# Kernel optimization log

Measured on AMD Instinct MI355X. Metric: run time of the kernel, lower is better.

## Reference

```python
import jax, jax.numpy as jnp
import numpy as np

N, S, E, H = 4, 1024, 768, 12
EPS = 1e-5


def layer_norm(x, g, b):
    m = jnp.mean(x, axis=-1, keepdims=True)
    v = jnp.mean((x - m) ** 2, axis=-1, keepdims=True)
    return (x - m) * jax.lax.rsqrt(v + EPS) * g + b


def setup_inputs() -> dict:
    key = jax.random.key(0)
    ks = jax.random.split(key, 18)
    s = 0.02
    return {
        "inputs": jax.random.normal(ks[0], (N, S, E), jnp.float32),
        "g1": jnp.ones((E,), jnp.float32),
        "b1": jnp.zeros((E,), jnp.float32),
        # per-head full-size projections: [H, E, E] (in->out layout)
        "Wq": jax.random.normal(ks[1], (H, E, E), jnp.float32) * s,
        "bq": jax.random.normal(ks[2], (H, E), jnp.float32) * s,
        "Wk": jax.random.normal(ks[3], (H, E, E), jnp.float32) * s,
        "bk": jax.random.normal(ks[4], (H, E), jnp.float32) * s,
        "Wv": jax.random.normal(ks[5], (H, E, E), jnp.float32) * s,
        "bv": jax.random.normal(ks[6], (H, E), jnp.float32) * s,
        "Wc": jax.random.normal(ks[7], (H * E, E), jnp.float32) * s,
        "bc": jax.random.normal(ks[8], (E,), jnp.float32) * s,
        "g2": jnp.ones((E,), jnp.float32),
        "b2": jnp.zeros((E,), jnp.float32),
        "Wfc": jax.random.normal(ks[9], (E, 4 * E), jnp.float32) * s,
        "bfc": jax.random.normal(ks[10], (4 * E,), jnp.float32) * s,
        "Wp": jax.random.normal(ks[11], (4 * E, E), jnp.float32) * s,
        "bp": jax.random.normal(ks[12], (E,), jnp.float32) * s,
    }


def reference(inputs, g1, b1, Wq, bq, Wk, bk, Wv, bv, Wc, bc, g2, b2, Wfc, bfc, Wp, bp):
    x = layer_norm(inputs, g1, b1)  # pre_norm output

    # batched per-head projections: [H, N, S, E]
    q = jnp.einsum('nse,hef->hnsf', x, Wq) + bq[:, None, None, :]
    k = jnp.einsum('nse,hef->hnsf', x, Wk) + bk[:, None, None, :]
    v = jnp.einsum('nse,hef->hnsf', x, Wv) + bv[:, None, None, :]

    # scores scaled by sqrt(n_embed) (as in the source), causal mask, softmax
    scores = jnp.einsum('hnsf,hntf->hnst', q, k) / jnp.sqrt(jnp.float32(E))
    causal = jnp.tril(jnp.ones((S, S), bool))
    scores = jnp.where(causal, scores, jnp.float32(-jnp.inf))
    attn = jax.nn.softmax(scores, axis=-1)
    heads = jnp.einsum('hnst,hntf->hnsf', attn, v)  # [H, N, S, E]

    # concat heads along feature dim -> [N, S, H*E], then c_proj
    cat = jnp.transpose(heads, (1, 2, 0, 3)).reshape(N, S, H * E)
    mha_out = cat @ Wc + bc

    # residual adds the NORMED input (as in the source)
    y = mha_out + x
    y2 = layer_norm(y, g2, b2)

    h = jax.nn.gelu(y2 @ Wfc + bfc, approximate=False)
    mlp_out = h @ Wp + bp
    return mlp_out + y2
```

## Files before the change

kernel.cpp:

```cpp
#include <hip/hip_runtime.h>
#include <hip/hip_bf16.h>
#include <math.h>


#define BM 128
#define BN 128
#define BK 64

typedef __attribute__((ext_vector_type(8))) short bf16x8;
typedef __attribute__((ext_vector_type(4))) float floatx4;

__device__ __forceinline__ short f2b(float f) {
  __hip_bfloat16 h = __float2bfloat16(f);
  return *reinterpret_cast<short*>(&h);
}
__device__ __forceinline__ float b2f(short s) {
  unsigned u = ((unsigned)(unsigned short)s) << 16;
  return __uint_as_float(u);
}

#if defined(__has_builtin)
#if __has_builtin(__builtin_amdgcn_global_load_lds)
#define HAS_GLLD 1
#endif
#endif

#ifdef HAS_GLLD
__device__ __forceinline__ void lds_dma16(const short* g, short* l) {
  __builtin_amdgcn_global_load_lds(
      (const __attribute__((address_space(1))) void*)g,
      (__attribute__((address_space(3))) void*)l, 16, 0, 0);
}
#endif

struct GP {
  const short* A; const short* B;
  long a_bs, b_bs;
  int lda, ldb;
  int a_kh; long a_hs;
  const float* bias0; const float* bias1; const float* bias2;
  short* C0; short* C1; short* C2;
  float* Cf;
  int ldc, zmod;
  long cz0, cz1, c_zs;
  int K, kchunk;
  float alpha;
  int zoff;
};

template<int MODE, int CAUSAL>
__device__ __forceinline__ void gemm_body(const GP& p)
{
  int bx = blockIdx.x;
  if (CAUSAL == 2) bx = gridDim.x - 1 - bx;
  const int m0 = bx * BM, n0 = blockIdx.y * BN;
  if (CAUSAL == 1 && n0 > m0 + (BM - 1)) return;
  const int z = blockIdx.z;
  const short* Ab = p.A + (size_t)z * p.a_bs;
  const short* Bb = p.B + (size_t)z * p.b_bs;
  int kbeg = 0, kend = p.K;
  if (p.kchunk) { kbeg = z * p.kchunk; kend = kbeg + p.kchunk; }
  if (CAUSAL == 2) { int lim = m0 + BM; if (lim < kend) kend = lim; }

  __shared__ __align__(16) short As[BM * BK];
  __shared__ __align__(16) short Bs[BN * BK];

  const int tid = threadIdx.x;
  const int lane = tid & 63, wave = tid >> 6;
  const int wm = (wave >> 1) * 64, wn = (wave & 1) * 64;
  const int l15 = lane & 15, quad = lane >> 4;
  const int rl = lane >> 3, pl = lane & 7;

  floatx4 acc[4][4];
#pragma unroll
  for (int i = 0; i < 4; i++)
#pragma unroll
    for (int j = 0; j < 4; j++) acc[i][j] = (floatx4){0.f, 0.f, 0.f, 0.f};

  const int cs = (pl - rl) & 7;

  for (int k0 = kbeg; k0 < kend; k0 += BK) {
    const short* Ak = Ab; int kb = k0;
    if (p.a_kh) { int h = k0 / p.a_kh; Ak = Ab + (size_t)h * p.a_hs; kb = k0 - h * p.a_kh; }
#pragma unroll
    for (int s = 0; s < 4; s++) {
      const int win = wave * 4 + s;
      const int row = win * 8 + rl;
      const short* ga = Ak + (size_t)(m0 + row) * p.lda + kb + cs * 8;
      const short* gb = Bb + (size_t)(n0 + row) * p.ldb + k0 + cs * 8;
#ifdef HAS_GLLD
      lds_dma16(ga, &As[win * 512]);
      lds_dma16(gb, &Bs[win * 512]);
#else
      *(int4*)&As[win * 512 + lane * 8] = *(const int4*)ga;
      *(int4*)&Bs[win * 512 + lane * 8] = *(const int4*)gb;
#endif
    }
    __syncthreads();
#pragma unroll
    for (int t = 0; t < 2; t++) {
      bf16x8 fa[4], fb[4];
#pragma unroll
      for (int i = 0; i < 4; i++) {
        const int ra = wm + i * 16 + l15;
        fa[i] = *(const bf16x8*)&As[ra * 64 + (((t << 2) + quad + ra) & 7) * 8];
        const int rb = wn + i * 16 + l15;
        fb[i] = *(const bf16x8*)&Bs[rb * 64 + (((t << 2) + quad + rb) & 7) * 8];
      }
#pragma unroll
      for (int i = 0; i < 4; i++)
#pragma unroll
        for (int j = 0; j < 4; j++)
          acc[i][j] = __builtin_amdgcn_mfma_f32_16x16x32_bf16(fa[i], fb[j], acc[i][j], 0, 0, 0);
    }
    __syncthreads();
  }

  const long coff = (long)(z % p.zmod) * p.cz0 + (long)(z / p.zmod) * p.cz1;
#pragma unroll
  for (int j = 0; j < 4; j++) {
    const int col = n0 + wn + j * 16 + l15;
    if constexpr (MODE == 0) {
#pragma unroll
      for (int i = 0; i < 4; i++) {
        const int rb = m0 + wm + i * 16 + quad * 4;
#pragma unroll
        for (int r = 0; r < 4; r++)
          p.C0[coff + (size_t)(rb + r) * p.ldc + col] = f2b(acc[i][j][r] * p.alpha);
      }
    } else if constexpr (MODE == 5) {
      const int part = (n0 + wn) / 768;
      const int cc = col - part * 768;
      const float* bp_ = (part == 0) ? p.bias0 : ((part == 1) ? p.bias1 : p.bias2);
      const float bvv = bp_[(p.zoff + z) * 768 + cc];
      if (part < 2) {
        short* dst = part ? p.C1 : p.C0;
#pragma unroll
        for (int i = 0; i < 4; i++) {
          const int rb = m0 + wm + i * 16 + quad * 4;
#pragma unroll
          for (int r = 0; r < 4; r++)
            dst[(size_t)z * p.c_zs + (size_t)(rb + r) * 768 + cc] = f2b(acc[i][j][r] + bvv);
        }
      } else {
#pragma unroll
        for (int i = 0; i < 4; i++) {
          const int rb = m0 + wm + i * 16 + quad * 4;
          short4 pk;
          pk.x = f2b(acc[i][j][0] + bvv);
          pk.y = f2b(acc[i][j][1] + bvv);
          pk.z = f2b(acc[i][j][2] + bvv);
          pk.w = f2b(acc[i][j][3] + bvv);
          const size_t addr = (((size_t)z * 4 + (rb >> 10)) * 768 + cc) * 1024 + (rb & 1023);
          *(short4*)&p.C2[addr] = pk;
        }
      }
    } else if constexpr (MODE == 4) {
#pragma unroll
      for (int i = 0; i < 4; i++) {
        const int rb = m0 + wm + i * 16 + quad * 4;
#pragma unroll
        for (int r = 0; r < 4; r++)
          p.Cf[(size_t)z * p.c_zs + (size_t)(rb + r) * p.ldc + col] = acc[i][j][r];
      }
    } else {
      const float bvv = p.bias0[col];
#pragma unroll
      for (int i = 0; i < 4; i++) {
        const int rb = m0 + wm + i * 16 + quad * 4;
#pragma unroll
        for (int r = 0; r < 4; r++) {
          float t = acc[i][j][r] + bvv;
          float u = 1.59576912160573071176f * t * (1.0f + 0.044715f * t * t);
          float gl = __fdividef(t, 1.0f + __expf(-u));
          p.C0[(size_t)(rb + r) * p.ldc + col] = f2b(gl);
        }
      }
    }
  }
}

__global__ void __launch_bounds__(256, 4) gemm_qkv(GP p)   { gemm_body<5, 0>(p); }
__global__ void __launch_bounds__(256, 4) gemm_sco(GP p)   { gemm_body<0, 1>(p); }
__global__ void __launch_bounds__(256, 4) gemm_pv(GP p)    { gemm_body<0, 2>(p); }
__global__ void __launch_bounds__(256, 4) gemm_cproj(GP p) { gemm_body<4, 0>(p); }
__global__ void __launch_bounds__(256, 4) gemm_fc(GP p)    { gemm_body<3, 0>(p); }
__global__ void __launch_bounds__(256, 4) gemm_mproj(GP p) { gemm_body<4, 0>(p); }

__global__ void __launch_bounds__(256) ln_kernel(
    const float* __restrict__ in, const float* __restrict__ g, const float* __restrict__ b,
    float* __restrict__ outf, short* __restrict__ outb)
{
  const long r = blockIdx.x;
  const float* x = in + r * 768;
  const int tid = threadIdx.x;
  float v0 = x[tid], v1 = x[tid + 256], v2 = x[tid + 512];
  float s = v0 + v1 + v2;
  float sq = v0 * v0 + v1 * v1 + v2 * v2;
  __shared__ float red[8];
  int lane = tid & 63, wave = tid >> 6;
#pragma unroll
  for (int o = 1; o < 64; o <<= 1) { s += __shfl_xor(s, o); sq += __shfl_xor(sq, o); }
  if (lane == 0) { red[wave] = s; red[4 + wave] = sq; }
  __syncthreads();
  s = red[0] + red[1] + red[2] + red[3];
  sq = red[4] + red[5] + red[6] + red[7];
  float mean = s * (1.0f / 768.0f);
  float var = sq * (1.0f / 768.0f) - mean * mean;
  float inv = rsqrtf(var + 1e-5f);
#pragma unroll
  for (int u = 0; u < 3; u++) {
    int c = tid + u * 256;
    float v = (u == 0) ? v0 : ((u == 1) ? v1 : v2);
    float y = (v - mean) * inv * g[c] + b[c];
    outf[r * 768 + c] = y;
    outb[r * 768 + c] = f2b(y);
  }
}

__global__ void __launch_bounds__(256) reduce_ln_kernel(
    const float* __restrict__ part, long pzs, int nsplit,
    const float* __restrict__ bias, const float* __restrict__ resid,
    const float* __restrict__ g, const float* __restrict__ b,
    float* __restrict__ outf, short* __restrict__ outb)
{
  const long r = blockIdx.x;
  const int tid = threadIdx.x;
  float y[3];
#pragma unroll
  for (int u = 0; u < 3; u++) {
    const int c = tid + u * 256;
    const size_t idx = (size_t)r * 768 + c;
    float s = part[idx];
    for (int zz = 1; zz < nsplit; zz++) s += part[(size_t)zz * pzs + idx];
    y[u] = s + bias[c] + resid[idx];
  }
  float s = y[0] + y[1] + y[2];
  float sq = y[0] * y[0] + y[1] * y[1] + y[2] * y[2];
  __shared__ float red[8];
  int lane = tid & 63, wave = tid >> 6;
#pragma unroll
  for (int o = 1; o < 64; o <<= 1) { s += __shfl_xor(s, o); sq += __shfl_xor(sq, o); }
  if (lane == 0) { red[wave] = s; red[4 + wave] = sq; }
  __syncthreads();
  s = red[0] + red[1] + red[2] + red[3];
  sq = red[4] + red[5] + red[6] + red[7];
  float mean = s * (1.0f / 768.0f);
  float var = sq * (1.0f / 768.0f) - mean * mean;
  float inv = rsqrtf(var + 1e-5f);
#pragma unroll
  for (int u = 0; u < 3; u++) {
    const int c = tid + u * 256;
    const float v = (y[u] - mean) * inv * g[c] + b[c];
    outf[(size_t)r * 768 + c] = v;
    outb[(size_t)r * 768 + c] = f2b(v);
  }
}

__global__ void __launch_bounds__(256) softmax_kernel(short* __restrict__ sc)
{
  const long gr = blockIdx.x;
  const int i = (int)(gr & 1023);
  short* row = sc + (gr >> 10) * (1024L * 1024) + (long)i * 1024;
  const int L = i + 1;
  const int tid = threadIdx.x;
  const int lane = tid & 63, wave = tid >> 6;
  __shared__ float red[4];
  float v[4];
  float mx = -3.0e38f;
#pragma unroll
  for (int s = 0; s < 4; s++) {
    int j = tid + s * 256;
    v[s] = (j < L) ? b2f(row[j]) : -3.0e38f;
    mx = fmaxf(mx, v[s]);
  }
#pragma unroll
  for (int o = 1; o < 64; o <<= 1) mx = fmaxf(mx, __shfl_xor(mx, o));
  if (lane == 0) red[wave] = mx;
  __syncthreads();
  mx = fmaxf(fmaxf(red[0], red[1]), fmaxf(red[2], red[3]));
  __syncthreads();
  float sum = 0.0f;
#pragma unroll
  for (int s = 0; s < 4; s++) {
    int j = tid + s * 256;
    if (j < L) { v[s] = __expf(v[s] - mx); sum += v[s]; }
  }
#pragma unroll
  for (int o = 1; o < 64; o <<= 1) sum += __shfl_xor(sum, o);
  if (lane == 0) red[wave] = sum;
  __syncthreads();
  sum = red[0] + red[1] + red[2] + red[3];
  float inv = 1.0f / sum;
#pragma unroll
  for (int s = 0; s < 4; s++) {
    int j = tid + s * 256;
    if (j < L) row[j] = f2b(v[s] * inv);
  }
  const int hi = i | 127;
  for (int j = L + tid; j <= hi; j += 256) row[j] = 0;
}

__global__ void __launch_bounds__(256) reduce_kernel(
    const float* __restrict__ part, long pzs, int nsplit,
    const float* __restrict__ bias, const float* __restrict__ resid,
    float* __restrict__ out)
{
  const size_t idx = ((size_t)blockIdx.x * 256 + threadIdx.x) * 4;
  float4 s = *(const float4*)&part[idx];
  for (int zz = 1; zz < nsplit; zz++) {
    float4 q = *(const float4*)&part[(size_t)zz * pzs + idx];
    s.x += q.x; s.y += q.y; s.z += q.z; s.w += q.w;
  }
  const int c = (int)(idx % 768);
  float4 b = *(const float4*)&bias[c];
  float4 r = *(const float4*)&resid[idx];
  *(float4*)&out[idx] = make_float4(s.x + b.x + r.x, s.y + b.y + r.y,
                                    s.z + b.z + r.z, s.w + b.w + r.w);
}

__global__ void __launch_bounds__(256) transpose_kernel(
    const float* __restrict__ W, short* __restrict__ Wt, int R, int C, long szs, long dzs)
{
  __shared__ float tile[32][33];
  const int c0 = blockIdx.x * 32, r0 = blockIdx.y * 32;
  const float* Wz = W + (size_t)blockIdx.z * szs;
  short* Wtz = Wt + (size_t)blockIdx.z * dzs;
  const int tx = threadIdx.x, ty = threadIdx.y;
#pragma unroll
  for (int i = 0; i < 32; i += 8)
    tile[ty + i][tx] = Wz[(size_t)(r0 + ty + i) * C + (c0 + tx)];
  __syncthreads();
#pragma unroll
  for (int i = 0; i < 32; i += 8)
    Wtz[(size_t)(c0 + ty + i) * R + (r0 + tx)] = f2b(tile[tx][ty + i]);
}

extern "C" void kernel_launch(void* const* d_in, const int* in_sizes, int n_in,
                              void* d_out, int out_size, void* d_ws, size_t ws_size,
                              hipStream_t stream)
{
  (void)in_sizes; (void)n_in; (void)out_size;
  const float* inputs = (const float*)d_in[0];
  const float* g1  = (const float*)d_in[1];
  const float* b1  = (const float*)d_in[2];
  const float* Wq  = (const float*)d_in[3];
  const float* bq  = (const float*)d_in[4];
  const float* Wk  = (const float*)d_in[5];
  const float* bk  = (const float*)d_in[6];
  const float* Wv  = (const float*)d_in[7];
  const float* bv  = (const float*)d_in[8];
  const float* Wc  = (const float*)d_in[9];
  const float* bc  = (const float*)d_in[10];
  const float* g2  = (const float*)d_in[11];
  const float* b2  = (const float*)d_in[12];
  const float* Wfc = (const float*)d_in[13];
  const float* bfc = (const float*)d_in[14];
  const float* Wp  = (const float*)d_in[15];
  const float* bp  = (const float*)d_in[16];
  float* out = (float*)d_out;

  const size_t NS = 4096, E = 768, S = 1024;

  char* base = (char*)d_ws;
  size_t off = 0;
  auto alloc = [&](size_t n) { char* r = base + off; off = (off + n + 255) & ~(size_t)255; return r; };

  float* x_f  = (float*)alloc(NS * E * 4);
  short* x_b  = (short*)alloc(NS * E * 2);
  short* Wqkv = (short*)alloc(12 * 3 * E * E * 2);
  short* WcT  = (short*)alloc(E * 9216 * 2);
  short* WfcT = (short*)alloc(3072 * E * 2);
  short* WpT  = (short*)alloc(E * 3072 * 2);
  short* cat  = (short*)alloc(12 * NS * E * 2);

  char* Rp = base + off;
  const size_t R_size = (ws_size > off) ? (ws_size - off) : 0;

  const size_t per_h = 3 * (NS * E * 2) + 4 * S * S * 2;
  static const int Gs[5] = {6, 4, 3, 2, 1};
  int G = 1;
  for (int i = 0; i < 5; i++)
    if ((size_t)Gs[i] * per_h <= R_size) { G = Gs[i]; break; }

  short* q_g  = (short*)Rp;
  short* k_g  = q_g + (size_t)G * NS * E;
  short* vT_g = k_g + (size_t)G * NS * E;
  short* sc_g = vT_g + (size_t)G * NS * E;

  size_t o2 = 0;
  float* partA = (float*)(Rp + o2); o2 += 4 * NS * E * 4;
  float* y2_f  = (float*)(Rp + o2); o2 += NS * E * 4;
  short* y2_b  = (short*)(Rp + o2); o2 += NS * E * 2;
  short* h_b   = (short*)(Rp + o2); o2 += NS * 3072 * 2;
  float* partB = (float*)cat;

  const dim3 tb(32, 8);
  transpose_kernel<<<dim3(24, 24, 12), tb, 0, stream>>>(Wq, Wqkv,         768, 768, (long)(E*E), (long)(3*E*E));
  transpose_kernel<<<dim3(24, 24, 12), tb, 0, stream>>>(Wk, Wqkv + E*E,   768, 768, (long)(E*E), (long)(3*E*E));
  transpose_kernel<<<dim3(24, 24, 12), tb, 0, stream>>>(Wv, Wqkv + 2*E*E, 768, 768, (long)(E*E), (long)(3*E*E));
  transpose_kernel<<<dim3(24, 288, 1), tb, 0, stream>>>(Wc, WcT, 9216, 768, 0, 0);
  transpose_kernel<<<dim3(96, 24, 1),  tb, 0, stream>>>(Wfc, WfcT, 768, 3072, 0, 0);
  transpose_kernel<<<dim3(24, 96, 1),  tb, 0, stream>>>(Wp, WpT, 3072, 768, 0, 0);

  ln_kernel<<<4096, 256, 0, stream>>>(inputs, g1, b1, x_f, x_b);

  const float sca = 0.03608439182435161f;
  for (int h0 = 0; h0 < 12; h0 += G) {
    {
      GP p{};
      p.A = x_b; p.lda = 768; p.a_bs = 0;
      p.B = Wqkv + (size_t)h0 * 3 * E * E; p.ldb = 768; p.b_bs = (long)(3 * E * E);
      p.bias0 = bq; p.bias1 = bk; p.bias2 = bv; p.zoff = h0;
      p.C0 = q_g; p.C1 = k_g; p.C2 = vT_g; p.c_zs = (long)(NS * E);
      p.ldc = 768; p.zmod = 1;
      p.K = 768; p.alpha = 1.0f;
      gemm_qkv<<<dim3(32, 18, G), 256, 0, stream>>>(p);
    }
    {
      GP p{};
      p.A = q_g; p.lda = 768; p.a_bs = (long)(S * E);
      p.B = k_g; p.ldb = 768; p.b_bs = (long)(S * E);
      p.C0 = sc_g; p.ldc = 1024; p.zmod = 1; p.cz0 = 0; p.cz1 = (long)(S * S);
      p.K = 768; p.alpha = sca;
      gemm_sco<<<dim3(8, 8, 4 * G), 256, 0, stream>>>(p);
    }
    softmax_kernel<<<4 * G * 1024, 256, 0, stream>>>(sc_g);
    {
      GP p{};
      p.A = sc_g; p.lda = 1024; p.a_bs = (long)(S * S);
      p.B = vT_g; p.ldb = 1024; p.b_bs = (long)(E * S);
      p.C0 = cat + (size_t)h0 * NS * E; p.ldc = 768;
      p.zmod = 4; p.cz0 = (long)(S * E); p.cz1 = (long)(NS * E);
      p.K = 1024; p.alpha = 1.0f;
      gemm_pv<<<dim3(8, 6, 4 * G), 256, 0, stream>>>(p);
    }
  }

  {
    GP p{};
    p.A = cat; p.lda = 768; p.a_kh = 768; p.a_hs = (long)(NS * E);
    p.B = WcT; p.ldb = 9216;
    p.Cf = partA; p.ldc = 768; p.c_zs = (long)(NS * E); p.zmod = 1;
    p.K = 9216; p.kchunk = 2304; p.alpha = 1.0f;
    gemm_cproj<<<dim3(32, 6, 4), 256, 0, stream>>>(p);
  }
  reduce_ln_kernel<<<4096, 256, 0, stream>>>(partA, (long)(NS * E), 4, bc, x_f,
                                             g2, b2, y2_f, y2_b);

  {
    GP p{};
    p.A = y2_b; p.lda = 768;
    p.B = WfcT; p.ldb = 768;
    p.bias0 = bfc; p.C0 = h_b; p.ldc = 3072; p.zmod = 1;
    p.K = 768; p.alpha = 1.0f;
    gemm_fc<<<dim3(32, 24, 1), 256, 0, stream>>>(p);
  }
  {
    GP p{};
    p.A = h_b; p.lda = 3072;
    p.B = WpT; p.ldb = 3072;
    p.Cf = partB; p.ldc = 768; p.c_zs = (long)(NS * E); p.zmod = 1;
    p.K = 3072; p.kchunk = 768; p.alpha = 1.0f;
    gemm_mproj<<<dim3(32, 6, 4), 256, 0, stream>>>(p);
  }
  reduce_kernel<<<3072, 256, 0, stream>>>(partB, (long)(NS * E), 4, bp, y2_f, out);
}
```

Baseline: 939.9 us.

## Fold Wq·Wkᵀ and Wv·Wc into precomputed weights to skip per-head Q/K/V projections

Rewrites attention algebraically. Scores become x·(Wq Wkᵀ)·xᵀ plus a row bias from bq·Wkᵀ·x, so the separate Q and K projections collapse into a single GEMM per head. Attention is applied directly to the transposed normed input, and Wv is folded into the c_proj weights along with bv into bc. This removes two of the three big per-head projection GEMMs and the V transpose. In exchange it adds weight-combining GEMMs, bias kernels, atomics, and bf16 rounding of the combined matrices, which can shift numerical accuracy.

```diff
diff --git a/kernel.cpp b/kernel.cpp
--- a/kernel.cpp
+++ b/kernel.cpp
@@ -38,10 +38,10 @@
   long a_bs, b_bs;
   int lda, ldb;
   int a_kh; long a_hs;
-  const float* bias0; const float* bias1; const float* bias2;
-  short* C0; short* C1; short* C2;
+  const float* bias0;
+  short* C0;
   float* Cf;
-  int ldc, zmod;
+  int ldc, zmod, b_zmod;
   long cz0, cz1, c_zs;
   int K, kchunk;
   float alpha;
@@ -57,7 +57,7 @@
   if (CAUSAL == 1 && n0 > m0 + (BM - 1)) return;
   const int z = blockIdx.z;
   const short* Ab = p.A + (size_t)z * p.a_bs;
-  const short* Bb = p.B + (size_t)z * p.b_bs;
+  const short* Bb = p.B + (size_t)(p.b_zmod ? (z % p.b_zmod) : z) * p.b_bs;
   int kbeg = 0, kend = p.K;
   if (p.kchunk) { kbeg = z * p.kchunk; kend = kbeg + p.kchunk; }
   if (CAUSAL == 2) { int lim = m0 + BM; if (lim < kend) kend = lim; }
@@ -128,32 +128,15 @@
         for (int r = 0; r < 4; r++)
           p.C0[coff + (size_t)(rb + r) * p.ldc + col] = f2b(acc[i][j][r] * p.alpha);
       }
-    } else if constexpr (MODE == 5) {
-      const int part = (n0 + wn) / 768;
-      const int cc = col - part * 768;
-      const float* bp_ = (part == 0) ? p.bias0 : ((part == 1) ? p.bias1 : p.bias2);
-      const float bvv = bp_[(p.zoff + z) * 768 + cc];
-      if (part < 2) {
-        short* dst = part ? p.C1 : p.C0;
-#pragma unroll
-        for (int i = 0; i < 4; i++) {
-          const int rb = m0 + wm + i * 16 + quad * 4;
-#pragma unroll
-          for (int r = 0; r < 4; r++)
-            dst[(size_t)z * p.c_zs + (size_t)(rb + r) * 768 + cc] = f2b(acc[i][j][r] + bvv);
-        }
-      } else {
-#pragma unroll
-        for (int i = 0; i < 4; i++) {
-          const int rb = m0 + wm + i * 16 + quad * 4;
-          short4 pk;
-          pk.x = f2b(acc[i][j][0] + bvv);
-          pk.y = f2b(acc[i][j][1] + bvv);
-          pk.z = f2b(acc[i][j][2] + bvv);
-          pk.w = f2b(acc[i][j][3] + bvv);
-          const size_t addr = (((size_t)z * 4 + (rb >> 10)) * 768 + cc) * 1024 + (rb & 1023);
-          *(short4*)&p.C2[addr] = pk;
-        }
+    } else if constexpr (MODE == 6) {
+      const float* bb = p.bias0 + ((size_t)(p.zoff + (z >> 2)) * 4096 + (size_t)(z & 3) * 1024);
+      const float bt = bb[col];
+#pragma unroll
+      for (int i = 0; i < 4; i++) {
+        const int rb = m0 + wm + i * 16 + quad * 4;
+#pragma unroll
+        for (int r = 0; r < 4; r++)
+          p.C0[coff + (size_t)(rb + r) * p.ldc + col] = f2b((acc[i][j][r] + bt) * p.alpha);
       }
     } else if constexpr (MODE == 4) {
 #pragma unroll
@@ -180,8 +163,9 @@
   }
 }
 
-__global__ void __launch_bounds__(256, 4) gemm_qkv(GP p)   { gemm_body<5, 0>(p); }
-__global__ void __launch_bounds__(256, 4) gemm_sco(GP p)   { gemm_body<0, 1>(p); }
+__global__ void __launch_bounds__(256, 4) gemm_pre(GP p)   { gemm_body<0, 0>(p); }
+__global__ void __launch_bounds__(256, 4) gemm_tmp(GP p)   { gemm_body<0, 0>(p); }
+__global__ void __launch_bounds__(256, 4) gemm_sco(GP p)   { gemm_body<6, 1>(p); }
 __global__ void __launch_bounds__(256, 4) gemm_pv(GP p)    { gemm_body<0, 2>(p); }
 __global__ void __launch_bounds__(256, 4) gemm_cproj(GP p) { gemm_body<4, 0>(p); }
 __global__ void __launch_bounds__(256, 4) gemm_fc(GP p)    { gemm_body<3, 0>(p); }
@@ -336,6 +320,70 @@
     Wtz[(size_t)(c0 + ty + i) * R + (r0 + tx)] = f2b(tile[tx][ty + i]);
 }
 
+__global__ void __launch_bounds__(256) cast_kernel(
+    const float* __restrict__ in, short* __restrict__ out, long n)
+{
+  const long i = ((long)blockIdx.x * 256 + threadIdx.x) * 4;
+  if (i < n) {
+    float4 v = *(const float4*)&in[i];
+    short4 o;
+    o.x = f2b(v.x); o.y = f2b(v.y); o.z = f2b(v.z); o.w = f2b(v.w);
+    *(short4*)&out[i] = o;
+  }
+}
+
+__global__ void __launch_bounds__(256) vw_kernel(
+    const float* __restrict__ Wk, const float* __restrict__ bq, float* __restrict__ vw)
+{
+  const int gid = blockIdx.x * 4 + (threadIdx.x >> 6);
+  const int lane = threadIdx.x & 63;
+  const int h = gid / 768;
+  const float* row = Wk + (size_t)gid * 768;
+  const float* bqh = bq + h * 768;
+  float s = 0.f;
+  for (int f = lane; f < 768; f += 64) s += row[f] * bqh[f];
+#pragma unroll
+  for (int o = 1; o < 64; o <<= 1) s += __shfl_xor(s, o);
+  if (lane == 0) vw[gid] = s;
+}
+
+__global__ void __launch_bounds__(256) bvec_kernel(
+    const float* __restrict__ x, const float* __restrict__ vw, float* __restrict__ bvec)
+{
+  const long r = blockIdx.x;
+  const float* xr = x + r * 768;
+  const int tid = threadIdx.x;
+  const float v0 = xr[tid], v1 = xr[tid + 256], v2 = xr[tid + 512];
+  __shared__ float red[4];
+  const int lane = tid & 63, wave = tid >> 6;
+  for (int h = 0; h < 12; h++) {
+    const float* w = vw + h * 768;
+    float s = v0 * w[tid] + v1 * w[tid + 256] + v2 * w[tid + 512];
+#pragma unroll
+    for (int o = 1; o < 64; o <<= 1) s += __shfl_xor(s, o);
+    if (lane == 0) red[wave] = s;
+    __syncthreads();
+    if (tid == 0) bvec[(size_t)h * 4096 + r] = red[0] + red[1] + red[2] + red[3];
+    __syncthreads();
+  }
+}
+
+__global__ void __launch_bounds__(256) bcv_init(const float* __restrict__ bc, float* __restrict__ bcv)
+{
+  const int j = blockIdx.x * 256 + threadIdx.x;
+  if (j < 768) bcv[j] = bc[j];
+}
+
+__global__ void __launch_bounds__(256) bcv_acc(
+    const float* __restrict__ Wc, const float* __restrict__ bv, float* __restrict__ bcv)
+{
+  const int j = blockIdx.x * 256 + threadIdx.x;
+  const int i0 = blockIdx.y * 256;
+  float s = 0.f;
+  for (int i = i0; i < i0 + 256; i++) s += bv[i] * Wc[(size_t)i * 768 + j];
+  atomicAdd(&bcv[j], s);
+}
+
 extern "C" void kernel_launch(void* const* d_in, const int* in_sizes, int n_in,
                               void* d_out, int out_size, void* d_ws, size_t ws_size,
                               hipStream_t stream)
@@ -347,7 +395,7 @@
   const float* Wq  = (const float*)d_in[3];
   const float* bq  = (const float*)d_in[4];
   const float* Wk  = (const float*)d_in[5];
-  const float* bk  = (const float*)d_in[6];
+  const float* bk  = (const float*)d_in[6];  (void)bk;
   const float* Wv  = (const float*)d_in[7];
   const float* bv  = (const float*)d_in[8];
   const float* Wc  = (const float*)d_in[9];
@@ -368,25 +416,31 @@
 
   float* x_f  = (float*)alloc(NS * E * 4);
   short* x_b  = (short*)alloc(NS * E * 2);
-  short* Wqkv = (short*)alloc(12 * 3 * E * E * 2);
+  short* xT   = (short*)alloc(NS * E * 2);
+  short* Mt   = (short*)alloc(12 * E * E * 2);
+  short* WvcT = (short*)alloc(E * 9216 * 2);
   short* WcT  = (short*)alloc(E * 9216 * 2);
   short* WfcT = (short*)alloc(3072 * E * 2);
   short* WpT  = (short*)alloc(E * 3072 * 2);
+  float* vw   = (float*)alloc(12 * E * 4);
+  float* bvec = (float*)alloc(12 * NS * 4);
+  float* bcv  = (float*)alloc(E * 4);
   short* cat  = (short*)alloc(12 * NS * E * 2);
 
   char* Rp = base + off;
   const size_t R_size = (ws_size > off) ? (ws_size - off) : 0;
 
-  const size_t per_h = 3 * (NS * E * 2) + 4 * S * S * 2;
+  short* Wq_c = (short*)Rp;
+  short* Wk_c = Wq_c + 12 * E * E;
+  short* Wv_c = Wk_c + 12 * E * E;
+
+  const size_t per_h = (NS * E * 2) + 4 * S * S * 2;
   static const int Gs[5] = {6, 4, 3, 2, 1};
   int G = 1;
   for (int i = 0; i < 5; i++)
     if ((size_t)Gs[i] * per_h <= R_size) { G = Gs[i]; break; }
-
-  short* q_g  = (short*)Rp;
-  short* k_g  = q_g + (size_t)G * NS * E;
-  short* vT_g = k_g + (size_t)G * NS * E;
-  short* sc_g = vT_g + (size_t)G * NS * E;
+  short* tmp_g = (short*)Rp;
+  short* sc_g  = tmp_g + (size_t)G * NS * E;
 
   size_t o2 = 0;
   float* partA = (float*)(Rp + o2); o2 += 4 * NS * E * 4;
@@ -396,31 +450,53 @@
   float* partB = (float*)cat;
 
   const dim3 tb(32, 8);
-  transpose_kernel<<<dim3(24, 24, 12), tb, 0, stream>>>(Wq, Wqkv,         768, 768, (long)(E*E), (long)(3*E*E));
-  transpose_kernel<<<dim3(24, 24, 12), tb, 0, stream>>>(Wk, Wqkv + E*E,   768, 768, (long)(E*E), (long)(3*E*E));
-  transpose_kernel<<<dim3(24, 24, 12), tb, 0, stream>>>(Wv, Wqkv + 2*E*E, 768, 768, (long)(E*E), (long)(3*E*E));
   transpose_kernel<<<dim3(24, 288, 1), tb, 0, stream>>>(Wc, WcT, 9216, 768, 0, 0);
   transpose_kernel<<<dim3(96, 24, 1),  tb, 0, stream>>>(Wfc, WfcT, 768, 3072, 0, 0);
   transpose_kernel<<<dim3(24, 96, 1),  tb, 0, stream>>>(Wp, WpT, 3072, 768, 0, 0);
+  const long WN = 12L * E * E;
+  cast_kernel<<<(WN / 4 + 255) / 256, 256, 0, stream>>>(Wq, Wq_c, WN);
+  cast_kernel<<<(WN / 4 + 255) / 256, 256, 0, stream>>>(Wk, Wk_c, WN);
+  cast_kernel<<<(WN / 4 + 255) / 256, 256, 0, stream>>>(Wv, Wv_c, WN);
+  {
+    GP p{};
+    p.A = Wk_c; p.lda = 768; p.a_bs = (long)(E * E);
+    p.B = Wq_c; p.ldb = 768; p.b_bs = (long)(E * E);
+    p.C0 = Mt; p.ldc = 768; p.zmod = 1; p.cz0 = 0; p.cz1 = (long)(E * E);
+    p.K = 768; p.alpha = 1.0f;
+    gemm_pre<<<dim3(6, 6, 12), 256, 0, stream>>>(p);
+  }
+  {
+    GP p{};
+    p.A = WcT; p.lda = 9216; p.a_bs = 768;
+    p.B = Wv_c; p.ldb = 768; p.b_bs = (long)(E * E);
+    p.C0 = WvcT; p.ldc = 9216; p.zmod = 1; p.cz0 = 0; p.cz1 = 768;
+    p.K = 768; p.alpha = 1.0f;
+    gemm_pre<<<dim3(6, 6, 12), 256, 0, stream>>>(p);
+  }
+  vw_kernel<<<2304, 256, 0, stream>>>(Wk, bq, vw);
+  bcv_init<<<3, 256, 0, stream>>>(bc, bcv);
+  bcv_acc<<<dim3(3, 36), 256, 0, stream>>>(Wc, bv, bcv);
 
   ln_kernel<<<4096, 256, 0, stream>>>(inputs, g1, b1, x_f, x_b);
+  transpose_kernel<<<dim3(24, 32, 4), tb, 0, stream>>>(x_f, xT, 1024, 768,
+                                                       (long)(S * E), (long)(E * S));
+  bvec_kernel<<<4096, 256, 0, stream>>>(x_f, vw, bvec);
 
   const float sca = 0.03608439182435161f;
   for (int h0 = 0; h0 < 12; h0 += G) {
     {
       GP p{};
       p.A = x_b; p.lda = 768; p.a_bs = 0;
-      p.B = Wqkv + (size_t)h0 * 3 * E * E; p.ldb = 768; p.b_bs = (long)(3 * E * E);
-      p.bias0 = bq; p.bias1 = bk; p.bias2 = bv; p.zoff = h0;
-      p.C0 = q_g; p.C1 = k_g; p.C2 = vT_g; p.c_zs = (long)(NS * E);
-      p.ldc = 768; p.zmod = 1;
+      p.B = Mt + (size_t)h0 * E * E; p.ldb = 768; p.b_bs = (long)(E * E);
+      p.C0 = tmp_g; p.ldc = 768; p.zmod = 1; p.cz0 = 0; p.cz1 = (long)(NS * E);
       p.K = 768; p.alpha = 1.0f;
-      gemm_qkv<<<dim3(32, 18, G), 256, 0, stream>>>(p);
+      gemm_tmp<<<dim3(32, 6, G), 256, 0, stream>>>(p);
     }
     {
       GP p{};
-      p.A = q_g; p.lda = 768; p.a_bs = (long)(S * E);
-      p.B = k_g; p.ldb = 768; p.b_bs = (long)(S * E);
+      p.A = tmp_g; p.lda = 768; p.a_bs = (long)(S * E);
+      p.B = x_b; p.ldb = 768; p.b_bs = (long)(S * E); p.b_zmod = 4;
+      p.bias0 = bvec; p.zoff = h0;
       p.C0 = sc_g; p.ldc = 1024; p.zmod = 1; p.cz0 = 0; p.cz1 = (long)(S * S);
       p.K = 768; p.alpha = sca;
       gemm_sco<<<dim3(8, 8, 4 * G), 256, 0, stream>>>(p);
@@ -429,7 +505,7 @@
     {
       GP p{};
       p.A = sc_g; p.lda = 1024; p.a_bs = (long)(S * S);
-      p.B = vT_g; p.ldb = 1024; p.b_bs = (long)(E * S);
+      p.B = xT; p.ldb = 1024; p.b_bs = (long)(E * S); p.b_zmod = 4;
       p.C0 = cat + (size_t)h0 * NS * E; p.ldc = 768;
       p.zmod = 4; p.cz0 = (long)(S * E); p.cz1 = (long)(NS * E);
       p.K = 1024; p.alpha = 1.0f;
@@ -440,12 +516,12 @@
   {
     GP p{};
     p.A = cat; p.lda = 768; p.a_kh = 768; p.a_hs = (long)(NS * E);
-    p.B = WcT; p.ldb = 9216;
+    p.B = WvcT; p.ldb = 9216;
     p.Cf = partA; p.ldc = 768; p.c_zs = (long)(NS * E); p.zmod = 1;
     p.K = 9216; p.kchunk = 2304; p.alpha = 1.0f;
     gemm_cproj<<<dim3(32, 6, 4), 256, 0, stream>>>(p);
   }
-  reduce_ln_kernel<<<4096, 256, 0, stream>>>(partA, (long)(NS * E), 4, bc, x_f,
+  reduce_ln_kernel<<<4096, 256, 0, stream>>>(partA, (long)(NS * E), 4, bcv, x_f,
                                              g2, b2, y2_f, y2_b);
 
   {
```

Measured after the change: 817.9 us. -13.0%, faster.
